# Optimization experiments

Measured on AMD Instinct MI355X. Metric: run time of the kernel, lower is better.

## Reference

```python
import jax, jax.numpy as jnp
import numpy as np

S, P = 64, 32          # scenes, pedestrians per scene (uniform)
N = S * P              # total pedestrians = 2048
H, E = 64, 64          # h_dim, embedding_dim
D1, D2 = 512, 1024     # mlp_pre_pool hidden, bottleneck_dim
EPS = 1e-5             # torch BatchNorm1d eps


def _batchnorm(x, gamma, beta):
    # Training-mode BN with per-scene batch stats (matches the per-scene
    # loop in the original, where BN sees one scene's num_ped^2 rows).
    # x: [S, P*P, D]
    mu = jnp.mean(x, axis=1, keepdims=True)
    var = jnp.mean(jnp.square(x - mu), axis=1, keepdims=True)  # biased var, as torch BN
    return (x - mu) * jax.lax.rsqrt(var + EPS) * gamma + beta


def setup_inputs() -> dict:
    key = jax.random.key(0)
    ks = jax.random.split(key, 16)
    h_states = jax.random.normal(ks[0], (1, N, H), jnp.float32)
    starts = jnp.arange(S, dtype=jnp.int32) * P
    seq_start_end = jnp.stack([starts, starts + P], axis=1)  # [S, 2]
    end_pos = jax.random.normal(ks[1], (N, 2), jnp.float32)
    rel_pos = jax.random.normal(ks[2], (N, 2), jnp.float32)  # unused (pooling_dim=2) but a fwd arg
    sc = 0.05
    params = dict(
        W_embed=jax.random.normal(ks[3], (2, E), jnp.float32) * sc,
        b_embed=jnp.zeros((E,), jnp.float32),
        W1=jax.random.normal(ks[4], (E + H, D1), jnp.float32) * sc,
        b1=jnp.zeros((D1,), jnp.float32),
        g1=jnp.ones((D1,), jnp.float32),
        be1=jnp.zeros((D1,), jnp.float32),
        W2=jax.random.normal(ks[5], (D1, D2), jnp.float32) * sc,
        b2=jnp.zeros((D2,), jnp.float32),
        g2=jnp.ones((D2,), jnp.float32),
        be2=jnp.zeros((D2,), jnp.float32),
    )
    return dict(h_states=h_states, seq_start_end=seq_start_end,
                end_pos=end_pos, rel_pos=rel_pos, **params)


def reference(h_states, seq_start_end, end_pos, rel_pos,
              W_embed, b_embed, W1, b1, g1, be1, W2, b2, g2, be2):
    # Uniform scenes: seq_start_end delimits S contiguous blocks of P peds.
    pos = end_pos.reshape(S, P, 2)
    h = h_states.reshape(N, H).reshape(S, P, H)
    # Original indexing: row (k*P + j) -> pos[j] - pos[k], hidden[j];
    # the final view(P, P, -1).max(1) maxes over j for each k.
    rel = pos[:, None, :, :] - pos[:, :, None, :]          # [S, Pk, Pj, 2]
    emb = rel @ W_embed + b_embed                          # [S, Pk, Pj, E]
    hid = jnp.broadcast_to(h[:, None, :, :], (S, P, P, H)) # hidden of j
    x = jnp.concatenate([emb, hid], axis=-1).reshape(S, P * P, E + H)
    x = jax.nn.relu(_batchnorm(x @ W1 + b1, g1, be1))      # [S, P*P, 512]
    x = jax.nn.relu(_batchnorm(x @ W2 + b2, g2, be2))      # [S, P*P, 1024]
    pool_h = x.reshape(S, P, P, D2).max(axis=2)            # max over j
    return pool_h.reshape(N, D2)
```

## Files before the change

### kernel.cpp

```cpp
#include <hip/hip_runtime.h>
#include <hip/hip_bf16.h>

#define S_ 64
#define P_ 32
#define N_ 2048
#define H_ 64
#define E_ 64
#define D1_ 512
#define D2_ 1024
#define EPS_ 1e-5f

typedef unsigned short u16;
using bf16x8 = __attribute__((ext_vector_type(8))) __bf16;
using floatx4 = __attribute__((ext_vector_type(4))) float;

__device__ inline u16 f2bf(float x) {
    unsigned u = __float_as_uint(x);
    unsigned r = (u + 0x7fffu + ((u >> 16) & 1u)) >> 16;
    return (u16)r;
}


__device__ void prep_scene_256(int u, int tid, float* smem,
                               const float* __restrict__ pos, const float* __restrict__ h,
                               const float* __restrict__ We, const float* __restrict__ W1,
                               const float* __restrict__ g1, const float* __restrict__ be1,
                               float* __restrict__ A, float* __restrict__ Bv) {
    const int s = u >> 2, dq = u & 3;
    const int jg = tid >> 7, dl = tid & 127;
    const int d = (dq << 7) + dl;
    float* hs = smem;
    float* ps = smem + 2048;
    float* red = smem + 2112;
    for (int i = tid; i < 2048; i += 256) hs[i] = h[(size_t)s * 2048 + i];
    if (tid < 64) ps[tid] = pos[s * 64 + tid];
    __syncthreads();
    float wq0 = 0.f, wq1 = 0.f;
    for (int e = 0; e < 64; ++e) {
        const float wv = W1[e * 512 + d];
        wq0 += We[e] * wv;
        wq1 += We[64 + e] * wv;
    }
    float w[16], uu[16];
#pragma unroll
    for (int jj = 0; jj < 16; ++jj) w[jj] = 0.f;
    const float4* h4 = (const float4*)hs;
    for (int e4 = 0; e4 < 16; ++e4) {
        const float c0 = W1[(64 + e4 * 4 + 0) * 512 + d];
        const float c1 = W1[(64 + e4 * 4 + 1) * 512 + d];
        const float c2 = W1[(64 + e4 * 4 + 2) * 512 + d];
        const float c3 = W1[(64 + e4 * 4 + 3) * 512 + d];
#pragma unroll
        for (int jj = 0; jj < 16; ++jj) {
            const float4 hv = h4[((jg << 4) + jj) * 16 + e4];
            w[jj] += hv.x * c0 + hv.y * c1 + hv.z * c2 + hv.w * c3;
        }
    }
    float sw = 0.f, sww = 0.f, su = 0.f, suu = 0.f;
#pragma unroll
    for (int jj = 0; jj < 16; ++jj) {
        const int j = (jg << 4) + jj;
        uu[jj] = ps[2 * j] * wq0 + ps[2 * j + 1] * wq1;
        w[jj] += uu[jj];
        sw += w[jj]; sww += w[jj] * w[jj];
        su += uu[jj]; suu += uu[jj] * uu[jj];
    }
    red[(jg << 7) + dl] = sw;
    red[256 + (jg << 7) + dl] = sww;
    red[512 + (jg << 7) + dl] = su;
    red[768 + (jg << 7) + dl] = suu;
    __syncthreads();
    const float tw = red[dl] + red[128 + dl];
    const float tww = red[256 + dl] + red[384 + dl];
    const float tu = red[512 + dl] + red[640 + dl];
    const float tuu = red[768 + dl] + red[896 + dl];
    const float mw = tw * (1.f / 32.f), mu2 = tu * (1.f / 32.f);
    const float var = (tww * (1.f / 32.f) - mw * mw) + (tuu * (1.f / 32.f) - mu2 * mu2);
    const float sc = rsqrtf(var + EPS_) * g1[d];
    const float bb = be1[d];
#pragma unroll
    for (int jj = 0; jj < 16; ++jj) {
        const int j = (jg << 4) + jj;
        A[(size_t)(s * 32 + j) * 512 + d] = (w[jj] - mw) * sc + bb;
        Bv[(size_t)(s * 32 + j) * 512 + d] = (uu[jj] - mu2) * sc;
    }
}

__device__ void w2t_tile_256(int b2, int tid, void* smem,
                             const float* __restrict__ W2, u16* __restrict__ w2t) {
    float (*tile)[65] = (float (*)[65])smem;
    const int bi = b2 & 15, bj = b2 >> 4;
    const int tx = tid & 63, ty = tid >> 6;
#pragma unroll
    for (int i = 0; i < 64; i += 4)
        tile[ty + i][tx] = W2[(size_t)(bj * 64 + ty + i) * 1024 + bi * 64 + tx];
    __syncthreads();
#pragma unroll
    for (int i = 0; i < 64; i += 4)
        w2t[(size_t)(bi * 64 + ty + i) * 512 + bj * 64 + tx] = f2bf(tile[tx][ty + i]);
}


__device__ __forceinline__ void ld4x4(float4 d[4], const float* __restrict__ p) {
    d[0] = *(const float4*)(p);
    d[1] = *(const float4*)(p + 4);
    d[2] = *(const float4*)(p + 8);
    d[3] = *(const float4*)(p + 12);
}

__device__ __forceinline__ void build_half(u16* __restrict__ AsN, int rowb,
                                           int posA, int posB,
                                           const float4 a[4], const float4 b[4]) {
    bf16x8 o;
    o[0] = (__bf16)fmaxf(a[0].x - b[0].x, 0.f);
    o[1] = (__bf16)fmaxf(a[0].y - b[0].y, 0.f);
    o[2] = (__bf16)fmaxf(a[0].z - b[0].z, 0.f);
    o[3] = (__bf16)fmaxf(a[0].w - b[0].w, 0.f);
    o[4] = (__bf16)fmaxf(a[1].x - b[1].x, 0.f);
    o[5] = (__bf16)fmaxf(a[1].y - b[1].y, 0.f);
    o[6] = (__bf16)fmaxf(a[1].z - b[1].z, 0.f);
    o[7] = (__bf16)fmaxf(a[1].w - b[1].w, 0.f);
    *(bf16x8*)(AsN + rowb + posA) = o;
    bf16x8 p;
    p[0] = (__bf16)fmaxf(a[2].x - b[2].x, 0.f);
    p[1] = (__bf16)fmaxf(a[2].y - b[2].y, 0.f);
    p[2] = (__bf16)fmaxf(a[2].z - b[2].z, 0.f);
    p[3] = (__bf16)fmaxf(a[2].w - b[2].w, 0.f);
    p[4] = (__bf16)fmaxf(a[3].x - b[3].x, 0.f);
    p[5] = (__bf16)fmaxf(a[3].y - b[3].y, 0.f);
    p[6] = (__bf16)fmaxf(a[3].z - b[3].z, 0.f);
    p[7] = (__bf16)fmaxf(a[3].w - b[3].w, 0.f);
    *(bf16x8*)(AsN + rowb + posB) = p;
}

__device__ __forceinline__ void stage_ws(const u16* __restrict__ w2t, u16* WsN,
                                         int N0, int kcol, int h, int wave,
                                         int lrow, int gchk) {
#pragma unroll
    for (int c = 0; c < 2; ++c) {
        const int rbase = h * 128 + wave * 16 + c * 8;
        const u16* gb = w2t + (size_t)(N0 + rbase + lrow) * 512 + kcol + gchk * 8;
        __builtin_amdgcn_global_load_lds(
            (const __attribute__((address_space(1))) void*)gb,
            (__attribute__((address_space(3))) void*)(WsN + rbase * 64), 16, 0, 0);
    }
}

template <int QM, int QN>
__device__ __forceinline__ void read_frags(bf16x8 af[4], bf16x8 wf[2],
                                           const u16* __restrict__ Ab,
                                           const u16* __restrict__ Wb,
                                           int wm, int wn, int l16, int pos) {
#pragma unroll
    for (int i = 0; i < 4; ++i)
        af[i] = *(const bf16x8*)(Ab + (wm * 128 + (QM * 4 + i) * 16 + l16) * 64 + pos);
#pragma unroll
    for (int n = 0; n < 2; ++n)
        wf[n] = *(const bf16x8*)(Wb + (wn * 64 + (QN * 2 + n) * 16 + l16) * 64 + pos);
}

template <int QM, int QN>
__device__ __forceinline__ void do_mfma(floatx4 (&acc)[8][4],
                                        const bf16x8 af[4], const bf16x8 wf[2]) {
#pragma unroll
    for (int i = 0; i < 4; ++i)
#pragma unroll
        for (int n = 0; n < 2; ++n)
            acc[QM * 4 + i][QN * 2 + n] = __builtin_amdgcn_mfma_f32_16x16x32_bf16(
                af[i], wf[n], acc[QM * 4 + i][QN * 2 + n], 0, 0, 0);
}

#define LGKM0() asm volatile("s_waitcnt lgkmcnt(0)" ::: "memory")
#define VM0()   asm volatile("s_waitcnt vmcnt(0)" ::: "memory")
#define VMC12() asm volatile("s_waitcnt vmcnt(12)" ::: "memory")

#define SANDWICH(QM, QN)                                              \
    __builtin_amdgcn_s_barrier();                                     \
    LGKM0();                                                          \
    __builtin_amdgcn_s_setprio(1);                                    \
    do_mfma<QM, QN>(acc, af, wf);                                     \
    read_frags<QM, QN>(af, wf, Ab, Wb, wm, wn, l16, posk1);           \
    do_mfma<QM, QN>(acc, af, wf);                                     \
    __builtin_amdgcn_s_setprio(0);                                    \
    __builtin_amdgcn_s_barrier();

__global__ __launch_bounds__(512, 2)
void k_gemm(const float* __restrict__ A, const float* __restrict__ Bv,
            const u16* __restrict__ w2t,
            float* __restrict__ maxv, float* __restrict__ minv,
            float* __restrict__ psum, float* __restrict__ psumsq) {
    extern __shared__ __align__(16) char lds_raw[];
    u16* AsB = (u16*)lds_raw;
    u16* WsB = AsB + 32768;

    const int tid = threadIdx.x;
    const int wave = tid >> 6, lane = tid & 63;
    const int wm = wave >> 2, wn = wave & 3;
    const int quad = lane >> 4, l16 = lane & 15;
    const int lrow = lane >> 3, gchk = (lane & 7) ^ lrow;

    const int bid = blockIdx.x;
    const int mb = bid >> 2, nb = bid & 3;
    const int s = mb >> 2, kq = mb & 3;
    const int N0 = nb << 8;

    const int brow = tid >> 2, kq4 = tid & 3;
    const int j0 = brow & 31, pl0 = brow >> 5;
    const float* Arow = A + ((size_t)(s * 32 + j0) << 9) + (kq4 << 4);
    const float* Brow0 = Bv + ((size_t)(s * 32 + kq * 8 + pl0) << 9) + (kq4 << 4);
    const float* Brow1 = Brow0 + (4 << 9);
    const int posA = ((kq4 * 2) ^ (brow & 7)) << 3;
    const int posB = ((kq4 * 2 + 1) ^ (brow & 7)) << 3;
    const int rowb0 = brow * 64;
    const int rowb1 = (128 + brow) * 64;

    const int posk0 = ((quad) ^ (l16 & 7)) << 3;
    const int posk1 = ((4 + quad) ^ (l16 & 7)) << 3;

    floatx4 acc[8][4] = {};
    float4 xa[4], xb[4], yb[4];

    {
        ld4x4(xa, Arow); ld4x4(xb, Brow0); ld4x4(yb, Brow1);
        stage_ws(w2t, WsB, N0, 0, 0, wave, lrow, gchk);
        stage_ws(w2t, WsB, N0, 0, 1, wave, lrow, gchk);
        build_half(AsB, rowb0, posA, posB, xa, xb);
        build_half(AsB, rowb1, posA, posB, xa, yb);
        ld4x4(xa, Arow + 64); ld4x4(xb, Brow0 + 64); ld4x4(yb, Brow1 + 64);
        VMC12();
        LGKM0();
        __builtin_amdgcn_s_barrier();
    }

    for (int t = 0; t < 8; ++t) {
        const int buf = t & 1;
        const u16* Ab = AsB + (buf << 14);
        const u16* Wb = WsB + (buf << 14);
        u16* AsN = AsB + ((buf ^ 1) << 14);
        u16* WsN = WsB + ((buf ^ 1) << 14);
        const bool pf = (t < 7);
        const int kn = (t + 1) << 6;
        bf16x8 af[4], wf[2];

        if (pf) {
            stage_ws(w2t, WsN, N0, kn, 0, wave, lrow, gchk);
            stage_ws(w2t, WsN, N0, kn, 1, wave, lrow, gchk);
        }
        read_frags<0, 0>(af, wf, Ab, Wb, wm, wn, l16, posk0);
        SANDWICH(0, 0)

        if (pf) build_half(AsN, rowb0, posA, posB, xa, xb);
        read_frags<0, 1>(af, wf, Ab, Wb, wm, wn, l16, posk0);
        SANDWICH(0, 1)

        if (pf) build_half(AsN, rowb1, posA, posB, xa, yb);
        read_frags<1, 0>(af, wf, Ab, Wb, wm, wn, l16, posk0);
        SANDWICH(1, 0)

        if (t < 6) {
            const int kn2 = (t + 2) << 6;
            ld4x4(xa, Arow + kn2); ld4x4(xb, Brow0 + kn2); ld4x4(yb, Brow1 + kn2);
            VMC12();
        } else {
            VM0();
        }
        read_frags<1, 1>(af, wf, Ab, Wb, wm, wn, l16, posk0);
        SANDWICH(1, 1)
    }

#pragma unroll
    for (int tn = 0; tn < 4; ++tn) {
        const int col = N0 + wn * 64 + tn * 16 + l16;
        float wsum = 0.f, wsq = 0.f;
#pragma unroll
        for (int e = 0; e < 4; ++e) {
            float vmax = -3.4e38f, vmin = 3.4e38f, vs = 0.f, vq = 0.f;
#pragma unroll
            for (int tm = e * 2; tm < e * 2 + 2; ++tm)
#pragma unroll
                for (int r = 0; r < 4; ++r) {
                    const float v = acc[tm][tn][r];
                    vmax = fmaxf(vmax, v);
                    vmin = fminf(vmin, v);
                    vs += v;
                    vq += v * v;
                }
#pragma unroll
            for (int off = 16; off < 64; off <<= 1) {
                vmax = fmaxf(vmax, __shfl_xor(vmax, off));
                vmin = fminf(vmin, __shfl_xor(vmin, off));
                vs += __shfl_xor(vs, off);
                vq += __shfl_xor(vq, off);
            }
            if (quad == 0) {
                const int kg = s * 32 + kq * 8 + wm * 4 + e;
                maxv[(size_t)kg * 1024 + col] = vmax;
                minv[(size_t)kg * 1024 + col] = vmin;
            }
            wsum += vs;
            wsq += vq;
        }
        if (quad == 0) {
            const int slot = ((s * 4 + kq) << 1) + wm;
            psum[(size_t)slot * 1024 + col] = wsum;
            psumsq[(size_t)slot * 1024 + col] = wsq;
        }
    }
}

__global__ __launch_bounds__(256)
void k_prep(const float* __restrict__ pos, const float* __restrict__ h,
            const float* __restrict__ We, const float* __restrict__ W1,
            const float* __restrict__ g1, const float* __restrict__ be1,
            const float* __restrict__ W2,
            float* __restrict__ A, float* __restrict__ Bv, u16* __restrict__ w2t) {
    __shared__ __align__(16) char smem_raw[16912];
    const int bid = blockIdx.x;
    if (bid < 256)
        prep_scene_256(bid, threadIdx.x, (float*)smem_raw, pos, h, We, W1, g1, be1, A, Bv);
    else
        w2t_tile_256(bid - 256, threadIdx.x, smem_raw, W2, w2t);
}

__global__ __launch_bounds__(256)
void k_final(const float* __restrict__ maxv, const float* __restrict__ minv,
             const float* __restrict__ psum, const float* __restrict__ psumsq,
             const float* __restrict__ g2, const float* __restrict__ be2,
             float* __restrict__ out) {
    const int u = blockIdx.x, tid = threadIdx.x;
    const int s3 = u >> 2;
    const int c = ((u & 3) << 8) + tid;
    float sm = 0.f, sq = 0.f;
#pragma unroll
    for (int t = 0; t < 8; ++t) {
        sm += psum[(size_t)(s3 * 8 + t) * 1024 + c];
        sq += psumsq[(size_t)(s3 * 8 + t) * 1024 + c];
    }
    const float mu = sm * (1.f / 1024.f);
    const float var = sq * (1.f / 1024.f) - mu * mu;
    const float inv = rsqrtf(var + EPS_);
    const float scale = g2[c] * inv;
    const float bb = be2[c];
    const float* src = (scale >= 0.f) ? maxv : minv;
    for (int k = 0; k < 32; ++k) {
        const float v = src[(size_t)(s3 * 32 + k) * 1024 + c];
        out[(size_t)(s3 * 32 + k) * 1024 + c] = fmaxf((v - mu) * scale + bb, 0.f);
    }
}

extern "C" void kernel_launch(void* const* d_in, const int* in_sizes, int n_in,
                              void* d_out, int out_size, void* d_ws, size_t ws_size,
                              hipStream_t stream) {
    const float* h_states = (const float*)d_in[0];
    const float* end_pos = (const float*)d_in[2];
    const float* W_embed = (const float*)d_in[4];
    const float* W1 = (const float*)d_in[6];
    const float* g1 = (const float*)d_in[8];
    const float* be1 = (const float*)d_in[9];
    const float* W2 = (const float*)d_in[10];
    const float* g2 = (const float*)d_in[12];
    const float* be2 = (const float*)d_in[13];
    float* out = (float*)d_out;

    float* Abuf = (float*)d_ws;
    float* Bbuf = Abuf + 1048576;
    float* maxv = Bbuf + 1048576;
    float* minv = maxv + 2097152;
    float* psum = minv + 2097152;
    float* psumsq = psum + 1048576;
    u16* w2t = (u16*)(psumsq + 1048576);

    static int lds_opt_in = 0;
    if (!lds_opt_in) {
        hipFuncSetAttribute(reinterpret_cast<const void*>(k_gemm),
                            hipFuncAttributeMaxDynamicSharedMemorySize, 131072);
        lds_opt_in = 1;
    }

    k_prep<<<dim3(384), dim3(256), 0, stream>>>(end_pos, h_states, W_embed, W1,
                                                g1, be1, W2, Abuf, Bbuf, w2t);
    k_gemm<<<dim3(1024), dim3(512), 131072, stream>>>(Abuf, Bbuf, w2t, maxv, minv,
                                                      psum, psumsq);
    k_final<<<dim3(256), dim3(256), 0, stream>>>(maxv, minv, psum, psumsq, g2, be2, out);
}
```

Baseline: 211.0 us.

## Restructure K-loop into two full-tile phases instead of four quadrant sandwiches

Each K-iteration changes from four quadrant sandwiches, each with two barriers and fragment reloads, to two phases, one per k-half (posk0, posk1). Each phase loads all 8 A and 4 W fragments, then issues 32 MFMAs. This halves the barrier count per iteration and adds a sched_barrier so MFMAs are not reordered across the wait. In exchange, register pressure rises (12 bf16x8 fragments live) under launch_bounds(512,2), and ds_read latency can no longer be interleaved with MFMAs inside a phase.

```diff
diff --git a/kernel.cpp b/kernel.cpp
--- a/kernel.cpp
+++ b/kernel.cpp
@@ -146,41 +146,38 @@
     }
 }
 
-template <int QM, int QN>
-__device__ __forceinline__ void read_frags(bf16x8 af[4], bf16x8 wf[2],
-                                           const u16* __restrict__ Ab,
-                                           const u16* __restrict__ Wb,
-                                           int wm, int wn, int l16, int pos) {
-#pragma unroll
-    for (int i = 0; i < 4; ++i)
-        af[i] = *(const bf16x8*)(Ab + (wm * 128 + (QM * 4 + i) * 16 + l16) * 64 + pos);
-#pragma unroll
-    for (int n = 0; n < 2; ++n)
-        wf[n] = *(const bf16x8*)(Wb + (wn * 64 + (QN * 2 + n) * 16 + l16) * 64 + pos);
-}
-
-template <int QM, int QN>
-__device__ __forceinline__ void do_mfma(floatx4 (&acc)[8][4],
-                                        const bf16x8 af[4], const bf16x8 wf[2]) {
-#pragma unroll
-    for (int i = 0; i < 4; ++i)
-#pragma unroll
-        for (int n = 0; n < 2; ++n)
-            acc[QM * 4 + i][QN * 2 + n] = __builtin_amdgcn_mfma_f32_16x16x32_bf16(
-                af[i], wf[n], acc[QM * 4 + i][QN * 2 + n], 0, 0, 0);
+__device__ __forceinline__ void read_all(bf16x8 af[8], bf16x8 wf[4],
+                                         const u16* __restrict__ Ab,
+                                         const u16* __restrict__ Wb,
+                                         int wm, int wn, int l16, int pos) {
+#pragma unroll
+    for (int i = 0; i < 8; ++i)
+        af[i] = *(const bf16x8*)(Ab + (wm * 128 + i * 16 + l16) * 64 + pos);
+#pragma unroll
+    for (int n = 0; n < 4; ++n)
+        wf[n] = *(const bf16x8*)(Wb + (wn * 64 + n * 16 + l16) * 64 + pos);
+}
+
+__device__ __forceinline__ void mfma_all(floatx4 (&acc)[8][4],
+                                         const bf16x8 af[8], const bf16x8 wf[4]) {
+#pragma unroll
+    for (int i = 0; i < 8; ++i)
+#pragma unroll
+        for (int n = 0; n < 4; ++n)
+            acc[i][n] = __builtin_amdgcn_mfma_f32_16x16x32_bf16(
+                af[i], wf[n], acc[i][n], 0, 0, 0);
 }
 
 #define LGKM0() asm volatile("s_waitcnt lgkmcnt(0)" ::: "memory")
 #define VM0()   asm volatile("s_waitcnt vmcnt(0)" ::: "memory")
 #define VMC12() asm volatile("s_waitcnt vmcnt(12)" ::: "memory")
 
-#define SANDWICH(QM, QN)                                              \
+#define PHASE_TAIL()                                                  \
     __builtin_amdgcn_s_barrier();                                     \
     LGKM0();                                                          \
+    __builtin_amdgcn_sched_barrier(0);                                \
     __builtin_amdgcn_s_setprio(1);                                    \
-    do_mfma<QM, QN>(acc, af, wf);                                     \
-    read_frags<QM, QN>(af, wf, Ab, Wb, wm, wn, l16, posk1);           \
-    do_mfma<QM, QN>(acc, af, wf);                                     \
+    mfma_all(acc, af, wf);                                            \
     __builtin_amdgcn_s_setprio(0);                                    \
     __builtin_amdgcn_s_barrier();
 
@@ -240,23 +237,18 @@
         u16* WsN = WsB + ((buf ^ 1) << 14);
         const bool pf = (t < 7);
         const int kn = (t + 1) << 6;
-        bf16x8 af[4], wf[2];
+        bf16x8 af[8], wf[4];
 
         if (pf) {
             stage_ws(w2t, WsN, N0, kn, 0, wave, lrow, gchk);
             stage_ws(w2t, WsN, N0, kn, 1, wave, lrow, gchk);
         }
-        read_frags<0, 0>(af, wf, Ab, Wb, wm, wn, l16, posk0);
-        SANDWICH(0, 0)
-
+        read_all(af, wf, Ab, Wb, wm, wn, l16, posk0);
         if (pf) build_half(AsN, rowb0, posA, posB, xa, xb);
-        read_frags<0, 1>(af, wf, Ab, Wb, wm, wn, l16, posk0);
-        SANDWICH(0, 1)
-
+        PHASE_TAIL()
+
+        read_all(af, wf, Ab, Wb, wm, wn, l16, posk1);
         if (pf) build_half(AsN, rowb1, posA, posB, xa, yb);
-        read_frags<1, 0>(af, wf, Ab, Wb, wm, wn, l16, posk0);
-        SANDWICH(1, 0)
-
         if (t < 6) {
             const int kn2 = (t + 2) << 6;
             ld4x4(xa, Arow + kn2); ld4x4(xb, Brow0 + kn2); ld4x4(yb, Brow1 + kn2);
@@ -264,8 +256,7 @@
         } else {
             VM0();
         }
-        read_frags<1, 1>(af, wf, Ab, Wb, wm, wn, l16, posk0);
-        SANDWICH(1, 1)
+        PHASE_TAIL()
     }
 
 #pragma unroll
```

New measurement: 213.7 us. No clear change (+1.3%).
